# Kernel optimization log

Measured on AMD Instinct MI355X. Metric: run time of the kernel, lower is better.

The kernel has to match this reference:

```python
import jax, jax.numpy as jnp
import numpy as np

H = 8  # num_heads
EPS = 1e-5

def _layernorm(x, g, b):
    mu = jnp.mean(x, axis=-1, keepdims=True)
    var = jnp.var(x, axis=-1, keepdims=True)
    return (x - mu) * jax.lax.rsqrt(var + EPS) * g + b

def setup_inputs() -> dict:
    key = jax.random.key(0)
    ks = jax.random.split(key, 16)
    B, S, D, F = 1, 4096, 512, 2048
    s = 1.0 / np.sqrt(D)
    inp = {
        'x': jax.random.normal(ks[0], (B, S, D), jnp.float32),
        'mask': jax.random.randint(ks[1], (S, S), 0, 2, jnp.int32),
        'wq': jax.random.normal(ks[2], (D, D), jnp.float32) * s,
        'bq': jnp.zeros((D,), jnp.float32),
        'wk': jax.random.normal(ks[3], (D, D), jnp.float32) * s,
        'bk': jnp.zeros((D,), jnp.float32),
        'wv': jax.random.normal(ks[4], (D, D), jnp.float32) * s,
        'bv': jnp.zeros((D,), jnp.float32),
        'wo': jax.random.normal(ks[5], (D, D), jnp.float32) * s,
        'bo': jnp.zeros((D,), jnp.float32),
        'w1': jax.random.normal(ks[6], (D, F), jnp.float32) * s,
        'b1': jnp.zeros((F,), jnp.float32),
        'w2': jax.random.normal(ks[7], (F, D), jnp.float32) * (1.0 / np.sqrt(F)),
        'b2': jnp.zeros((D,), jnp.float32),
        'g1': jnp.ones((D,), jnp.float32),
        'be1': jnp.zeros((D,), jnp.float32),
        'g2': jnp.ones((D,), jnp.float32),
        'be2': jnp.zeros((D,), jnp.float32),
    }
    return inp

def reference(x, mask, wq, bq, wk, bk, wv, bv, wo, bo, w1, b1, w2, b2, g1, be1, g2, be2):
    B, S, D = x.shape
    Dh = D // H

    def split(t):  # (B,S,D) -> (B,H,S,Dh)
        return t.reshape(B, S, H, Dh).transpose(0, 2, 1, 3)

    q = split(x @ wq + bq)
    k = split(x @ wk + bk)
    v = split(x @ wv + bv)

    # naive attention: full (B,H,S,S) scores, NO 1/sqrt(Dh) scaling (faithful to source)
    scores = jnp.einsum('bhsd,bhtd->bhst', q, k)
    scores = jnp.where(mask == 0, jnp.float32(-1e9), scores)
    attn = jax.nn.softmax(scores, axis=-1)
    out = jnp.einsum('bhst,bhtd->bhsd', attn, v)
    out = out.transpose(0, 2, 1, 3).reshape(B, S, D) @ wo + bo

    x = _layernorm(x + out, g1, be1)  # dropout is identity at inference
    ff = jax.nn.relu(x @ w1 + b1) @ w2 + b2
    x = _layernorm(x + ff, g2, be2)
    return x
```

## Files before the change

kernel.cpp:

```cpp
#include <hip/hip_runtime.h>

typedef unsigned short u16;
typedef unsigned int u32;
typedef unsigned long long u64;
typedef __attribute__((ext_vector_type(4))) float f32x4;
typedef __attribute__((ext_vector_type(8))) short bf16x8;
typedef __attribute__((ext_vector_type(4))) u16 u16x4;
typedef __attribute__((ext_vector_type(2))) u32 u32x2;

#define DEV __device__ __forceinline__

DEV u16 f2bf(float f) {
  union { float f; u32 u; } c; c.f = f;
  u32 u = c.u;
  u += 0x7fffu + ((u >> 16) & 1u);
  return (u16)(u >> 16);
}
DEV float bf2f(u16 h) {
  union { u32 u; float f; } c; c.u = ((u32)h) << 16;
  return c.f;
}
DEV u32 fbits(float f) { union { float f; u32 u; } c; c.f = f; return c.u; }
DEV u32 packtrunc(float a, float b) {
  return (fbits(b) & 0xFFFF0000u) | (fbits(a) >> 16);
}

DEV void gload_lds16(const void* g, void* l) {
  __builtin_amdgcn_global_load_lds(
      (const __attribute__((address_space(1))) u32*)(u64)g,
      (__attribute__((address_space(3))) u32*)(u32)(u64)l,
      16, 0, 0);
}

struct PrepW { const float* w; u16* th; u16* tl; int R, C, gxmask, gxshift; };
struct PrepArgs {
  const float* x; u16* xh; u16* xl;
  const int* mask; unsigned long long* mbits;
  PrepW pw[6];
};

__global__ __launch_bounds__(256) void prep(PrepArgs a) {
  __shared__ float t[32][33];
  int b = blockIdx.x, tid = threadIdx.x;
  if (b < 2048) {
    int i = (b * 256 + tid) * 4;
    f32x4 v = *(const f32x4*)(a.x + i);
    u16x4 h, l;
#pragma unroll
    for (int j = 0; j < 4; ++j) { h[j] = f2bf(v[j]); l[j] = f2bf(v[j] - bf2f(h[j])); }
    *(u16x4*)(a.xh + i) = h;
    *(u16x4*)(a.xl + i) = l;
    return;
  }
  b -= 2048;
  if (b < 3072) {
    int wi, base;
    if (b < 1024) { wi = b >> 8; base = b & 255; }
    else if (b < 2048) { wi = 4; base = b - 1024; }
    else { wi = 5; base = b - 2048; }
    PrepW p = a.pw[wi];
    int c0 = (base & p.gxmask) * 32, r0 = (base >> p.gxshift) * 32;
    int tx = tid & 31, ty = tid >> 5;
#pragma unroll
    for (int i = 0; i < 4; ++i)
      t[ty + 8 * i][tx] = p.w[(size_t)(r0 + ty + 8 * i) * p.C + c0 + tx];
    __syncthreads();
#pragma unroll
    for (int i = 0; i < 4; ++i) {
      float v = t[tx][ty + 8 * i];
      u16 h = f2bf(v);
      size_t o = (size_t)(c0 + ty + 8 * i) * p.R + r0 + tx;
      p.th[o] = h;
      if (p.tl) p.tl[o] = f2bf(v - bf2f(h));
    }
    return;
  }
  b -= 3072;
  size_t i = (size_t)b * 256 + tid;
  unsigned long long bb = __ballot(a.mask[i] != 0);
  if ((tid & 63) == 0) a.mbits[i >> 6] = bb;
}

struct QkvArgs {
  const u16 *Ah, *Al;
  const u16 *Bh[3];
  const float* bias[3];
  u16 *Qh, *Kh, *Vt;
};

__global__ __launch_bounds__(256) void gemm_qkv(QkvArgs a) {
  const int K = 512;
  const float L2E = 1.44269504088896340736f;
  const int z = blockIdx.z;
  const u16* __restrict__ Bh = a.Bh[z];
  const float* __restrict__ bias = a.bias[z];
  const int bn = blockIdx.x * 128, bm = blockIdx.y * 128;
  const int tid = threadIdx.x;
  const int wave = tid >> 6, lane = tid & 63;
  const int l16 = lane & 15, quad = lane >> 4;
  const int wm = (wave >> 1) * 64, wn = (wave & 1) * 64;

  __shared__ u16 sA[2][128 * 32];
  __shared__ u16 sAl[2][128 * 32];
  __shared__ u16 sB[2][128 * 32];

  const int srow = wave * 32 + (lane >> 2);
  const int scol = (lane & 3) * 8;
  const u16* srcA0 = a.Ah + (size_t)(bm + srow) * K + scol;
  const u16* srcAl0 = a.Al + (size_t)(bm + srow) * K + scol;
  const u16* srcB0 = Bh + (size_t)(bn + srow) * K + scol;
  const size_t half_off = (size_t)16 * K;

  auto prefetchG = [&](int kt, int buf) {
    u16* dA = sA[buf] + wave * 1024;
    u16* dAl = sAl[buf] + wave * 1024;
    u16* dB = sB[buf] + wave * 1024;
    gload_lds16(srcA0 + kt, dA);
    gload_lds16(srcA0 + half_off + kt, dA + 512);
    gload_lds16(srcAl0 + kt, dAl);
    gload_lds16(srcAl0 + half_off + kt, dAl + 512);
    gload_lds16(srcB0 + kt, dB);
    gload_lds16(srcB0 + half_off + kt, dB + 512);
  };

  f32x4 acc[4][4] = {};
  prefetchG(0, 0);

  for (int i = 0; i < 16; ++i) {
    __syncthreads();
    if (i + 1 < 16) prefetchG((i + 1) << 5, (i + 1) & 1);
    const u16* bufA = sA[i & 1];
    const u16* bufAl = sAl[i & 1];
    const u16* bufB = sB[i & 1];

    bf16x8 a_h[4], a_l[4], b_h[4];
#pragma unroll
    for (int mt = 0; mt < 4; ++mt) {
      a_h[mt] = *(const bf16x8*)(bufA + (wm + mt * 16 + l16) * 32 + quad * 8);
      a_l[mt] = *(const bf16x8*)(bufAl + (wm + mt * 16 + l16) * 32 + quad * 8);
    }
#pragma unroll
    for (int nt = 0; nt < 4; ++nt)
      b_h[nt] = *(const bf16x8*)(bufB + (wn + nt * 16 + l16) * 32 + quad * 8);
#pragma unroll
    for (int mt = 0; mt < 4; ++mt)
#pragma unroll
      for (int nt = 0; nt < 4; ++nt) {
        acc[mt][nt] = __builtin_amdgcn_mfma_f32_16x16x32_bf16(a_h[mt], b_h[nt], acc[mt][nt], 0, 0, 0);
        acc[mt][nt] = __builtin_amdgcn_mfma_f32_16x16x32_bf16(a_l[mt], b_h[nt], acc[mt][nt], 0, 0, 0);
      }
  }

  if (z == 2) {
#pragma unroll
    for (int nt = 0; nt < 4; ++nt) {
      int col = bn + wn + nt * 16 + l16;
      float bv = bias[col];
#pragma unroll
      for (int mt = 0; mt < 4; ++mt) {
        int row0 = bm + wm + mt * 16 + quad * 4;
        u16x4 o;
#pragma unroll
        for (int r = 0; r < 4; ++r) o[r] = f2bf(acc[mt][nt][r] + bv);
        *(u16x4*)(a.Vt + (size_t)col * 4096 + row0) = o;
      }
    }
  } else {
    u16* __restrict__ C = (z == 0) ? a.Qh : a.Kh;
    float scale = (z == 0) ? L2E : 1.f;
#pragma unroll
    for (int mt = 0; mt < 4; ++mt)
#pragma unroll
      for (int nt = 0; nt < 4; ++nt) {
        int col = bn + wn + nt * 16 + l16;
        float bv = bias[col];
#pragma unroll
        for (int r = 0; r < 4; ++r) {
          int row = bm + wm + mt * 16 + quad * 4 + r;
          C[(size_t)row * 512 + col] = f2bf((acc[mt][nt][r] + bv) * scale);
        }
      }
  }
}

template <int RELU, int BF16OUT>
__global__ __launch_bounds__(256) void gemm_bt(const u16* __restrict__ Ah,
                                               const u16* __restrict__ Bh,
                                               const float* __restrict__ bias,
                                               float* __restrict__ Cf,
                                               u16* __restrict__ Ch,
                                               int N, int K) {
  const int bn = blockIdx.x * 128, bm = blockIdx.y * 128;
  const int tid = threadIdx.x;
  const int wave = tid >> 6, lane = tid & 63;
  const int l16 = lane & 15, quad = lane >> 4;
  const int wm = (wave >> 1) * 64, wn = (wave & 1) * 64;

  __shared__ u16 sA[2][128 * 32];
  __shared__ u16 sB[2][128 * 32];

  const int srow = wave * 32 + (lane >> 2);
  const int scol = (lane & 3) * 8;
  const u16* srcA0 = Ah + (size_t)(bm + srow) * K + scol;
  const u16* srcB0 = Bh + (size_t)(bn + srow) * K + scol;
  const size_t half_off = (size_t)16 * K;

  auto prefetchG = [&](int kt, int buf) {
    u16* dA = sA[buf] + wave * 1024;
    u16* dB = sB[buf] + wave * 1024;
    gload_lds16(srcA0 + kt, dA);
    gload_lds16(srcA0 + half_off + kt, dA + 512);
    gload_lds16(srcB0 + kt, dB);
    gload_lds16(srcB0 + half_off + kt, dB + 512);
  };

  f32x4 acc[4][4] = {};
  prefetchG(0, 0);

  const int steps = K >> 5;
  for (int i = 0; i < steps; ++i) {
    __syncthreads();
    if (i + 1 < steps) prefetchG((i + 1) << 5, (i + 1) & 1);
    const u16* bufA = sA[i & 1];
    const u16* bufB = sB[i & 1];

    bf16x8 a_h[4], b_h[4];
#pragma unroll
    for (int mt = 0; mt < 4; ++mt)
      a_h[mt] = *(const bf16x8*)(bufA + (wm + mt * 16 + l16) * 32 + quad * 8);
#pragma unroll
    for (int nt = 0; nt < 4; ++nt)
      b_h[nt] = *(const bf16x8*)(bufB + (wn + nt * 16 + l16) * 32 + quad * 8);
#pragma unroll
    for (int mt = 0; mt < 4; ++mt)
#pragma unroll
      for (int nt = 0; nt < 4; ++nt)
        acc[mt][nt] = __builtin_amdgcn_mfma_f32_16x16x32_bf16(a_h[mt], b_h[nt], acc[mt][nt], 0, 0, 0);
  }

#pragma unroll
  for (int mt = 0; mt < 4; ++mt)
#pragma unroll
    for (int nt = 0; nt < 4; ++nt) {
      int col = bn + wn + nt * 16 + l16;
      float bv = bias ? bias[col] : 0.f;
#pragma unroll
      for (int r = 0; r < 4; ++r) {
        int row = bm + wm + mt * 16 + quad * 4 + r;
        float v = acc[mt][nt][r] + bv;
        if (RELU) v = fmaxf(v, 0.f);
        size_t oidx = (size_t)row * N + col;
        if (BF16OUT) Ch[oidx] = f2bf(v);
        else Cf[oidx] = v;
      }
    }
}

struct AttnIO { float* O[4]; float* lp; };

__global__ __launch_bounds__(256) void attn(const u16* __restrict__ Qh,
                                            const u16* __restrict__ Kh,
                                            const u16* __restrict__ Vt,
                                            const u64* __restrict__ mb64,
                                            AttnIO io) {
  const int S = 4096, D = 512;
  const int h = blockIdx.x >> 2, chunk = blockIdx.x & 3;
  const int tid = threadIdx.x, wave = tid >> 6, lane = tid & 63;
  const int l16 = lane & 15, quad = lane >> 4;
  const int q0w = blockIdx.y * 128 + wave * 32;
  const int kbeg = chunk * 1024;
  const int sw = l16 & 7;

  __shared__ u16 sK[64 * 64];
  __shared__ u16 sV[2][64 * 64];
  __shared__ u16 sP[4][32 * 40];
  u16* myP = &sP[wave][0];

  const int skey = lane >> 3;
  const int sch  = lane & 7;
  const u16* srcK = Kh + (size_t)(kbeg + wave * 8 + skey) * D + h * 64 + ((sch ^ skey) * 8);
  const u16* srcV = Vt + (size_t)(h * 64 + wave * 8 + skey) * S + kbeg + ((sch ^ skey) * 8);
  u16* dstK = sK + wave * 512;

  auto stageK = [&](int it) {
    const u16* p = srcK + (size_t)it * 64 * D;
    gload_lds16(p, dstK);
    gload_lds16(p + (size_t)32 * D, dstK + 32 * 64);
  };
  auto stageV = [&](int it) {
    const u16* p = srcV + it * 64;
    u16* d = sV[it & 1] + wave * 512;
    gload_lds16(p, d);
    gload_lds16(p + (size_t)32 * S, d + 32 * 64);
  };

  bf16x8 qf[2][2];
#pragma unroll
  for (int qt = 0; qt < 2; ++qt)
#pragma unroll
    for (int kd = 0; kd < 2; ++kd)
      qf[qt][kd] = *(const bf16x8*)(Qh + (size_t)(q0w + qt * 16 + l16) * D + h * 64 + kd * 32 + quad * 8);

  f32x4 accO[2][4] = {};
  float l_lane[2] = {0.f, 0.f};
  const int wbase = kbeg >> 6;

  stageV(0);
  stageK(0);
  u64 wmCur[2];
#pragma unroll
  for (int qt = 0; qt < 2; ++qt)
    wmCur[qt] = mb64[(size_t)(q0w + qt * 16 + l16) * 64 + wbase];

  for (int it = 0; it < 16; ++it) {
    __syncthreads();
    if (it + 1 < 16) stageV(it + 1);
    u64 wmNext[2] = {0, 0};
    if (it + 1 < 16) {
#pragma unroll
      for (int qt = 0; qt < 2; ++qt)
        wmNext[qt] = mb64[(size_t)(q0w + qt * 16 + l16) * 64 + wbase + it + 1];
    }

    f32x4 sc[4][2];
#pragma unroll
    for (int kt4 = 0; kt4 < 4; ++kt4) {
      const u16* arow = sK + (kt4 * 16 + l16) * 64;
      bf16x8 ka0 = *(const bf16x8*)(arow + ((quad ^ sw) * 8));
      bf16x8 ka1 = *(const bf16x8*)(arow + (((4 + quad) ^ sw) * 8));
#pragma unroll
      for (int qt = 0; qt < 2; ++qt) {
        f32x4 s = {};
        s = __builtin_amdgcn_mfma_f32_16x16x32_bf16(ka0, qf[qt][0], s, 0, 0, 0);
        s = __builtin_amdgcn_mfma_f32_16x16x32_bf16(ka1, qf[qt][1], s, 0, 0, 0);
        sc[kt4][qt] = s;
      }
    }
#pragma unroll
    for (int k2 = 0; k2 < 2; ++k2) {
      const int baseb = k2 * 16 + quad * 4;
#pragma unroll
      for (int qt = 0; qt < 2; ++qt) {
        float p[4];
#pragma unroll
        for (int r = 0; r < 4; ++r) {
          bool keep = (wmCur[qt] >> (baseb + r)) & 1ull;
          p[r] = exp2f(keep ? sc[k2][qt][r] : -1e9f);
        }
        l_lane[qt] += (p[0] + p[1]) + (p[2] + p[3]);
        u32x2 pk = {packtrunc(p[0], p[1]), packtrunc(p[2], p[3])};
        *(u32x2*)(myP + (qt * 16 + l16) * 40 + k2 * 16 + quad * 4) = pk;
      }
    }
    __syncthreads();
    if (it + 1 < 16) stageK(it + 1);
    const u16* bV = sV[it & 1];

    {
      bf16x8 pa[2];
#pragma unroll
      for (int qt = 0; qt < 2; ++qt)
        pa[qt] = *(const bf16x8*)(myP + (qt * 16 + l16) * 40 + quad * 8);
#pragma unroll
      for (int nt = 0; nt < 4; ++nt) {
        bf16x8 vf = *(const bf16x8*)(bV + (nt * 16 + l16) * 64 + ((quad ^ sw) * 8));
#pragma unroll
        for (int qt = 0; qt < 2; ++qt)
          accO[qt][nt] = __builtin_amdgcn_mfma_f32_16x16x32_bf16(pa[qt], vf, accO[qt][nt], 0, 0, 0);
      }
    }
#pragma unroll
    for (int k2 = 0; k2 < 2; ++k2) {
      const int baseb = 32 + k2 * 16 + quad * 4;
#pragma unroll
      for (int qt = 0; qt < 2; ++qt) {
        float p[4];
#pragma unroll
        for (int r = 0; r < 4; ++r) {
          bool keep = (wmCur[qt] >> (baseb + r)) & 1ull;
          p[r] = exp2f(keep ? sc[2 + k2][qt][r] : -1e9f);
        }
        l_lane[qt] += (p[0] + p[1]) + (p[2] + p[3]);
        u32x2 pk = {packtrunc(p[0], p[1]), packtrunc(p[2], p[3])};
        *(u32x2*)(myP + (qt * 16 + l16) * 40 + k2 * 16 + quad * 4) = pk;
      }
    }
    {
      bf16x8 pa[2];
#pragma unroll
      for (int qt = 0; qt < 2; ++qt)
        pa[qt] = *(const bf16x8*)(myP + (qt * 16 + l16) * 40 + quad * 8);
#pragma unroll
      for (int nt = 0; nt < 4; ++nt) {
        bf16x8 vf = *(const bf16x8*)(bV + (nt * 16 + l16) * 64 + (((4 + quad) ^ sw) * 8));
#pragma unroll
        for (int qt = 0; qt < 2; ++qt)
          accO[qt][nt] = __builtin_amdgcn_mfma_f32_16x16x32_bf16(pa[qt], vf, accO[qt][nt], 0, 0, 0);
      }
    }
    wmCur[0] = wmNext[0];
    wmCur[1] = wmNext[1];
  }

#pragma unroll
  for (int qt = 0; qt < 2; ++qt) {
    float s = l_lane[qt];
    s += __shfl_xor(s, 16);
    s += __shfl_xor(s, 32);
    l_lane[qt] = s;
  }
  float* Op = io.O[chunk];
#pragma unroll
  for (int qt = 0; qt < 2; ++qt)
#pragma unroll
    for (int nt = 0; nt < 4; ++nt)
#pragma unroll
      for (int r = 0; r < 4; ++r) {
        int row = q0w + qt * 16 + quad * 4 + r;
        Op[((size_t)h * S + row) * 64 + nt * 16 + l16] = accO[qt][nt][r];
      }
  if (quad == 0)
#pragma unroll
    for (int qt = 0; qt < 2; ++qt)
      io.lp[((size_t)h * 4 + chunk) * S + q0w + qt * 16 + l16] = l_lane[qt];
}

__global__ __launch_bounds__(256) void attn_combine(AttnIO io, u16* __restrict__ ctx) {
  const int S = 4096;
  int i = (blockIdx.x * 256 + threadIdx.x);
  int row = i >> 7;
  int col4 = (i & 127) * 4;
  int h = col4 >> 6, c = col4 & 63;
  size_t ob = ((size_t)h * S + row) * 64 + c;
  f32x4 o = {0.f, 0.f, 0.f, 0.f};
  float l = 0.f;
#pragma unroll
  for (int p = 0; p < 4; ++p) {
    o += *(const f32x4*)(io.O[p] + ob);
    l += io.lp[((size_t)h * 4 + p) * S + row];
  }
  float rl = 1.f / l;
  u16x4 out;
#pragma unroll
  for (int j = 0; j < 4; ++j) out[j] = f2bf(o[j] * rl);
  *(u16x4*)(ctx + (size_t)row * 512 + col4) = out;
}

__global__ __launch_bounds__(256) void resid_ln(const float* __restrict__ X,
                                                const float* __restrict__ Y,
                                                const float* __restrict__ g,
                                                const float* __restrict__ b,
                                                float* __restrict__ outF,
                                                u16* __restrict__ outH) {
  int row = blockIdx.x * 4 + (int)(threadIdx.x >> 6);
  int lane = threadIdx.x & 63;
  const float* x0 = X + (size_t)row * 512;
  const float* y0 = Y + (size_t)row * 512;
  int c0 = lane * 4, c1 = 256 + lane * 4;
  f32x4 v0 = *(const f32x4*)(x0 + c0) + *(const f32x4*)(y0 + c0);
  f32x4 v1 = *(const f32x4*)(x0 + c1) + *(const f32x4*)(y0 + c1);
  float s = 0.f, s2 = 0.f;
#pragma unroll
  for (int j = 0; j < 4; ++j) {
    s += v0[j] + v1[j];
    s2 += v0[j] * v0[j] + v1[j] * v1[j];
  }
#pragma unroll
  for (int m = 1; m < 64; m <<= 1) {
    s += __shfl_xor(s, m);
    s2 += __shfl_xor(s2, m);
  }
  float mean = s * (1.f / 512.f);
  float var = s2 * (1.f / 512.f) - mean * mean;
  float rs = rsqrtf(var + 1e-5f);
  f32x4 o0, o1;
#pragma unroll
  for (int j = 0; j < 4; ++j) {
    o0[j] = (v0[j] - mean) * rs * g[c0 + j] + b[c0 + j];
    o1[j] = (v1[j] - mean) * rs * g[c1 + j] + b[c1 + j];
  }
  if (outF) {
    *(f32x4*)(outF + (size_t)row * 512 + c0) = o0;
    *(f32x4*)(outF + (size_t)row * 512 + c1) = o1;
  }
  if (outH) {
    u16x4 h0, h1;
#pragma unroll
    for (int j = 0; j < 4; ++j) { h0[j] = f2bf(o0[j]); h1[j] = f2bf(o1[j]); }
    *(u16x4*)(outH + (size_t)row * 512 + c0) = h0;
    *(u16x4*)(outH + (size_t)row * 512 + c1) = h1;
  }
}

extern "C" void kernel_launch(void* const* d_in, const int* in_sizes, int n_in,
                              void* d_out, int out_size, void* d_ws, size_t ws_size,
                              hipStream_t stream) {
  (void)in_sizes; (void)n_in; (void)out_size; (void)ws_size;
  const float* x   = (const float*)d_in[0];
  const int*   mask= (const int*)d_in[1];
  const float* wq  = (const float*)d_in[2];
  const float* bq  = (const float*)d_in[3];
  const float* wk  = (const float*)d_in[4];
  const float* bk  = (const float*)d_in[5];
  const float* wv  = (const float*)d_in[6];
  const float* bv  = (const float*)d_in[7];
  const float* wo  = (const float*)d_in[8];
  const float* bo  = (const float*)d_in[9];
  const float* w1  = (const float*)d_in[10];
  const float* b1  = (const float*)d_in[11];
  const float* w2  = (const float*)d_in[12];
  const float* b2  = (const float*)d_in[13];
  const float* g1  = (const float*)d_in[14];
  const float* be1 = (const float*)d_in[15];
  const float* g2  = (const float*)d_in[16];
  const float* be2 = (const float*)d_in[17];

  const int S = 4096, D = 512, F = 2048;
  char* ws = (char*)d_ws;
  size_t cur = 0;
  auto alloc = [&](size_t bytes) {
    char* p = ws + cur;
    cur += (bytes + 255) & ~(size_t)255;
    return p;
  };
  u16* wqT = (u16*)alloc((size_t)D * D * 2);
  u16* wkT = (u16*)alloc((size_t)D * D * 2);
  u16* wvT = (u16*)alloc((size_t)D * D * 2);
  u16* woT = (u16*)alloc((size_t)D * D * 2);
  u16* w1T = (u16*)alloc((size_t)D * F * 2);
  u16* w2T = (u16*)alloc((size_t)D * F * 2);
  u32* mbits = (u32*)alloc((size_t)S * S / 8);
  u16* xh = (u16*)alloc((size_t)S * D * 2);
  u16* xl = (u16*)alloc((size_t)S * D * 2);
  u16* Qh = (u16*)alloc((size_t)S * D * 2);
  u16* Kh = (u16*)alloc((size_t)S * D * 2);
  u16* Vt = (u16*)alloc((size_t)S * D * 2);
  u16* hx = (u16*)alloc((size_t)S * D * 2); (void)hx;
  u16* ctx = (u16*)alloc((size_t)S * D * 2);
  float* x1 = (float*)alloc((size_t)S * D * 4);
  u16* x1h = (u16*)alloc((size_t)S * D * 2);
  float* Oex = (float*)alloc((size_t)2 * S * D * 4);
  AttnIO io;
  io.O[0] = (float*)xh;
  io.O[1] = x1;
  io.O[2] = Oex;
  io.O[3] = Oex + (size_t)S * D;
  io.lp = (float*)x1h;
  float* proj = (float*)xh;
  u16* hbuf = Qh;
  float* ff2 = Oex;

  PrepArgs pa;
  pa.x = x; pa.xh = xh; pa.xl = xl;
  pa.mask = mask; pa.mbits = (unsigned long long*)mbits;
  pa.pw[0] = {wq, wqT, nullptr, D, D, 15, 4};
  pa.pw[1] = {wk, wkT, nullptr, D, D, 15, 4};
  pa.pw[2] = {wv, wvT, nullptr, D, D, 15, 4};
  pa.pw[3] = {wo, woT, nullptr, D, D, 15, 4};
  pa.pw[4] = {w1, w1T, nullptr, D, F, 63, 6};
  pa.pw[5] = {w2, w2T, nullptr, F, D, 15, 4};

  QkvArgs qa;
  qa.Ah = xh; qa.Al = xl;
  qa.Bh[0] = wqT; qa.Bh[1] = wkT; qa.Bh[2] = wvT;
  qa.bias[0] = bq; qa.bias[1] = bk; qa.bias[2] = bv;
  qa.Qh = Qh; qa.Kh = Kh; qa.Vt = Vt;

  prep<<<70656, 256, 0, stream>>>(pa);
  gemm_qkv<<<dim3(4, 32, 3), 256, 0, stream>>>(qa);
  attn<<<dim3(32, 32), 256, 0, stream>>>(Qh, Kh, Vt, (const u64*)mbits, io);
  attn_combine<<<(S * D / 4) / 256, 256, 0, stream>>>(io, ctx);
  gemm_bt<0, 0><<<dim3(4, 32), 256, 0, stream>>>(ctx, woT, bo, proj, nullptr, D, D);
  resid_ln<<<S / 4, 256, 0, stream>>>(x, proj, g1, be1, x1, x1h);
  gemm_bt<1, 1><<<dim3(16, 32), 256, 0, stream>>>(x1h, w1T, b1, nullptr, hbuf, F, D);
  gemm_bt<0, 0><<<dim3(4, 32), 256, 0, stream>>>(hbuf, w2T, b2, ff2, nullptr, D, F);
  resid_ln<<<S / 4, 256, 0, stream>>>(x1, ff2, g2, be2, (float*)d_out, nullptr);
}
```

Measured before the change: 340.5 us.

## Split-K the output and FFN2 GEMMs, summing partials in residual layernorm

The two N=512 GEMMs (out-projection and second FFN layer) now split K in two across blockIdx.z. This doubles the grid from 128 to 256 blocks so more compute units stay busy. Each half writes a separate fp32 partial, and the residual layernorm kernel reads and adds the second partial, which costs extra global memory traffic. The attention kernel also pre-shifts the 64-bit mask words into two 32-bit halves per iteration, reducing 64-bit shift work in the inner loop.

```diff
diff --git a/kernel.cpp b/kernel.cpp
--- a/kernel.cpp
+++ b/kernel.cpp
@@ -183,13 +183,17 @@
   }
 }
 
-template <int RELU, int BF16OUT>
+template <int RELU, int BF16OUT, int NSPLIT>
 __global__ __launch_bounds__(256) void gemm_bt(const u16* __restrict__ Ah,
                                                const u16* __restrict__ Bh,
                                                const float* __restrict__ bias,
                                                float* __restrict__ Cf,
+                                               float* __restrict__ Cf2,
                                                u16* __restrict__ Ch,
                                                int N, int K) {
+  const int z = (NSPLIT > 1) ? blockIdx.z : 0;
+  const int Ksub = K / NSPLIT;
+  const int kbeg = z * Ksub;
   const int bn = blockIdx.x * 128, bm = blockIdx.y * 128;
   const int tid = threadIdx.x;
   const int wave = tid >> 6, lane = tid & 63;
@@ -201,8 +205,8 @@
 
   const int srow = wave * 32 + (lane >> 2);
   const int scol = (lane & 3) * 8;
-  const u16* srcA0 = Ah + (size_t)(bm + srow) * K + scol;
-  const u16* srcB0 = Bh + (size_t)(bn + srow) * K + scol;
+  const u16* srcA0 = Ah + (size_t)(bm + srow) * K + kbeg + scol;
+  const u16* srcB0 = Bh + (size_t)(bn + srow) * K + kbeg + scol;
   const size_t half_off = (size_t)16 * K;
 
   auto prefetchG = [&](int kt, int buf) {
@@ -217,7 +221,7 @@
   f32x4 acc[4][4] = {};
   prefetchG(0, 0);
 
-  const int steps = K >> 5;
+  const int steps = Ksub >> 5;
   for (int i = 0; i < steps; ++i) {
     __syncthreads();
     if (i + 1 < steps) prefetchG((i + 1) << 5, (i + 1) & 1);
@@ -238,12 +242,13 @@
         acc[mt][nt] = __builtin_amdgcn_mfma_f32_16x16x32_bf16(a_h[mt], b_h[nt], acc[mt][nt], 0, 0, 0);
   }
 
+  float* __restrict__ Co = (NSPLIT > 1 && z == 1) ? Cf2 : Cf;
 #pragma unroll
   for (int mt = 0; mt < 4; ++mt)
 #pragma unroll
     for (int nt = 0; nt < 4; ++nt) {
       int col = bn + wn + nt * 16 + l16;
-      float bv = bias ? bias[col] : 0.f;
+      float bv = (bias && z == 0) ? bias[col] : 0.f;
 #pragma unroll
       for (int r = 0; r < 4; ++r) {
         int row = bm + wm + mt * 16 + quad * 4 + r;
@@ -251,7 +256,7 @@
         if (RELU) v = fmaxf(v, 0.f);
         size_t oidx = (size_t)row * N + col;
         if (BF16OUT) Ch[oidx] = f2bf(v);
-        else Cf[oidx] = v;
+        else Co[oidx] = v;
       }
     }
 }
@@ -321,6 +326,12 @@
       for (int qt = 0; qt < 2; ++qt)
         wmNext[qt] = mb64[(size_t)(q0w + qt * 16 + l16) * 64 + wbase + it + 1];
     }
+    u32 wlo[2], whi[2];
+#pragma unroll
+    for (int qt = 0; qt < 2; ++qt) {
+      wlo[qt] = (u32)(wmCur[qt] >> (quad * 4));
+      whi[qt] = (u32)(wmCur[qt] >> (quad * 4 + 32));
+    }
 
     f32x4 sc[4][2];
 #pragma unroll
@@ -338,13 +349,12 @@
     }
 #pragma unroll
     for (int k2 = 0; k2 < 2; ++k2) {
-      const int baseb = k2 * 16 + quad * 4;
 #pragma unroll
       for (int qt = 0; qt < 2; ++qt) {
         float p[4];
 #pragma unroll
         for (int r = 0; r < 4; ++r) {
-          bool keep = (wmCur[qt] >> (baseb + r)) & 1ull;
+          bool keep = (wlo[qt] >> (k2 * 16 + r)) & 1u;
           p[r] = exp2f(keep ? sc[k2][qt][r] : -1e9f);
         }
         l_lane[qt] += (p[0] + p[1]) + (p[2] + p[3]);
@@ -371,13 +381,12 @@
     }
 #pragma unroll
     for (int k2 = 0; k2 < 2; ++k2) {
-      const int baseb = 32 + k2 * 16 + quad * 4;
 #pragma unroll
       for (int qt = 0; qt < 2; ++qt) {
         float p[4];
 #pragma unroll
         for (int r = 0; r < 4; ++r) {
-          bool keep = (wmCur[qt] >> (baseb + r)) & 1ull;
+          bool keep = (whi[qt] >> (k2 * 16 + r)) & 1u;
           p[r] = exp2f(keep ? sc[2 + k2][qt][r] : -1e9f);
         }
         l_lane[qt] += (p[0] + p[1]) + (p[2] + p[3]);
@@ -448,6 +457,7 @@
 
 __global__ __launch_bounds__(256) void resid_ln(const float* __restrict__ X,
                                                 const float* __restrict__ Y,
+                                                const float* __restrict__ Y2,
                                                 const float* __restrict__ g,
                                                 const float* __restrict__ b,
                                                 float* __restrict__ outF,
@@ -459,6 +469,11 @@
   int c0 = lane * 4, c1 = 256 + lane * 4;
   f32x4 v0 = *(const f32x4*)(x0 + c0) + *(const f32x4*)(y0 + c0);
   f32x4 v1 = *(const f32x4*)(x0 + c1) + *(const f32x4*)(y0 + c1);
+  if (Y2) {
+    const float* y2 = Y2 + (size_t)row * 512;
+    v0 += *(const f32x4*)(y2 + c0);
+    v1 += *(const f32x4*)(y2 + c1);
+  }
   float s = 0.f, s2 = 0.f;
 #pragma unroll
   for (int j = 0; j < 4; ++j) {
@@ -547,8 +562,10 @@
   io.O[3] = Oex + (size_t)S * D;
   io.lp = (float*)x1h;
   float* proj = (float*)xh;
+  float* projB = Oex + (size_t)S * D;
   u16* hbuf = Qh;
   float* ff2 = Oex;
+  float* ff2B = Oex + (size_t)S * D;
 
   PrepArgs pa;
   pa.x = x; pa.xh = xh; pa.xl = xl;
@@ -570,9 +587,9 @@
   gemm_qkv<<<dim3(4, 32, 3), 256, 0, stream>>>(qa);
   attn<<<dim3(32, 32), 256, 0, stream>>>(Qh, Kh, Vt, (const u64*)mbits, io);
   attn_combine<<<(S * D / 4) / 256, 256, 0, stream>>>(io, ctx);
-  gemm_bt<0, 0><<<dim3(4, 32), 256, 0, stream>>>(ctx, woT, bo, proj, nullptr, D, D);
-  resid_ln<<<S / 4, 256, 0, stream>>>(x, proj, g1, be1, x1, x1h);
-  gemm_bt<1, 1><<<dim3(16, 32), 256, 0, stream>>>(x1h, w1T, b1, nullptr, hbuf, F, D);
-  gemm_bt<0, 0><<<dim3(4, 32), 256, 0, stream>>>(hbuf, w2T, b2, ff2, nullptr, D, F);
-  resid_ln<<<S / 4, 256, 0, stream>>>(x1, ff2, g2, be2, (float*)d_out, nullptr);
-}
+  gemm_bt<0, 0, 2><<<dim3(4, 32, 2), 256, 0, stream>>>(ctx, woT, bo, proj, projB, nullptr, D, D);
+  resid_ln<<<S / 4, 256, 0, stream>>>(x, proj, projB, g1, be1, x1, x1h);
+  gemm_bt<1, 1, 1><<<dim3(16, 32), 256, 0, stream>>>(x1h, w1T, b1, nullptr, nullptr, hbuf, F, D);
+  gemm_bt<0, 0, 2><<<dim3(4, 32, 2), 256, 0, stream>>>(hbuf, w2T, b2, ff2, ff2B, nullptr, D, F);
+  resid_ln<<<S / 4, 256, 0, stream>>>(x1, ff2, ff2B, g2, be2, (float*)d_out, nullptr);
+}
```

After: 322.7 us. -5.2%, faster.
